# Kernel tuning notes

Hardware: AMD Instinct MI355X
Metric: run time of the kernel (lower is better)

Reference implementation:

```python
import jax, jax.numpy as jnp
import numpy as np
from jax.scipy.special import logsumexp

WORD_DIM = 512
SCRF_DIM = 256
N_TAGS = 12
ALLOWED_SPAN = 8
START_ID = 10
STOP_ID = 11
SEQ_LEN = 768
N_SPANS = 96


def _compute_scores(h, Wl, bl, Wr, br, Gl, bgl, Gr, bgr, Wt, bt, transitions):
    # h: [1, L, D] already projected by Dense
    Lc, D = h.shape[1], h.shape[2]
    scores = jnp.zeros((1, Lc, Lc, D), h.dtype)
    diag = jnp.arange(Lc)
    ht = h
    scores = scores.at[:, diag, diag].set(ht)
    for sl in range(1, min(ALLOWED_SPAN, Lc)):
        l, r = ht[:, :-1], ht[:, 1:]
        h_hat = 4.0 * jax.nn.sigmoid(l @ Wl.T + bl + r @ Wr.T + br) - 2.0
        # exp/normalize over 3 gates == softmax over gate axis
        g = (l @ Gl.T + bgl + r @ Gr.T + bgr).reshape(1, Lc - sl, 3, D)
        wgt = jax.nn.softmax(g, axis=2)
        ht = wgt[:, :, 0] * h_hat + wgt[:, :, 1] * l + wgt[:, :, 2] * r
        scores = scores.at[:, diag[:Lc - sl], diag[sl:]].set(ht)
    tagsc = scores @ Wt.T + bt  # [1, L, L, T]
    # final[b,i,j,prev,tag] = tagsc[b,i,j,tag] + transitions[prev,tag]
    return tagsc[:, :, :, None, :] + transitions[None, None, None]


def _forward_pass(s5):
    # s5: [1, L, L, T, T]; semi-Markov forward algorithm, windows of width <= ALLOWED_SPAN
    Lc, T = s5.shape[1], s5.shape[3]
    A = ALLOWED_SPAN
    i0 = jnp.arange(1, Lc + 1)
    k = jnp.arange(A)
    p = i0[:, None] - A + k[None, :]              # candidate span-start positions [L, A]
    m = p >= 0                                    # valid window mask (istarts = max(0, i-A))
    x = s5[0][jnp.clip(p, 0), (i0 - 1)[:, None]]  # [L, A, T, T] span scores ending at i-1
    buf0 = jnp.full((A, T), -10000.0, s5.dtype).at[A - 1, START_ID].set(0.0)

    def step(buf, inp):
        xi, mi = inp
        # tmp[k, prev, tag] = score + logalpha[start, prev]
        tmp = jnp.where(mi[:, None, None], xi + buf[:, :, None], -1e30)
        na = logsumexp(tmp, axis=(0, 1))  # [T]
        return jnp.concatenate([buf[1:], na[None]], axis=0), na

    _, alphas = jax.lax.scan(step, buf0, (x, m))
    return alphas[-1, :STOP_ID].sum()


def _gold_score(s5, tags):
    Lc, T = s5.shape[1], s5.shape[3]
    gf = tags[:, :, 0] * (Lc * T * T) + tags[:, :, 1] * (T * T) + tags[:, :, 2] * T + tags[:, :, 3]
    return jnp.take_along_axis(s5.reshape(1, -1), gf, axis=1).sum()


def setup_inputs() -> dict:
    key = jax.random.key(0)
    ks = jax.random.split(key, 16)
    D, W3 = SCRF_DIM, 3 * SCRF_DIM
    s = 0.05
    def w(k, shape):
        return jax.random.normal(k, shape, dtype=jnp.float32) * s
    return {
        "feats": jax.random.normal(ks[0], (1, SEQ_LEN, WORD_DIM), dtype=jnp.float32),
        "tags": jax.random.randint(ks[1], (1, N_SPANS, 4), 0, N_TAGS),
        "Wd": w(ks[2], (D, WORD_DIM)), "bd": jnp.zeros((D,), jnp.float32),
        "Wl": w(ks[3], (D, D)), "bl": jnp.zeros((D,), jnp.float32),
        "Wr": w(ks[4], (D, D)), "br": jnp.zeros((D,), jnp.float32),
        "Gl": w(ks[5], (W3, D)), "bgl": jnp.zeros((W3,), jnp.float32),
        "Gr": w(ks[6], (W3, D)), "bgr": jnp.zeros((W3,), jnp.float32),
        "Wt": w(ks[7], (N_TAGS, D)), "bt": jnp.zeros((N_TAGS,), jnp.float32),
        "transitions": w(ks[8], (N_TAGS, N_TAGS)),
    }


def reference(feats, tags, Wd, bd, Wl, bl, Wr, br, Gl, bgl, Gr, bgr, Wt, bt, transitions):
    h = feats @ Wd.T + bd  # Dense: word_dim -> scrf_dim
    s5 = _compute_scores(h, Wl, bl, Wr, br, Gl, bgl, Gr, bgr, Wt, bt, transitions)
    gold = _gold_score(s5, tags)
    logZ = _forward_pass(s5)
    return logZ - gold
```

## Files before the change

### kernel.cpp

```cpp
#include <hip/hip_runtime.h>

typedef __attribute__((ext_vector_type(8))) short short8;
typedef __attribute__((ext_vector_type(4))) float f32x4;

#define TPAD 100
#define BARSTRIDE 512

__device__ __forceinline__ float bf2f(short s) {
  return __uint_as_float(((unsigned)(unsigned short)s) << 16);
}
__device__ __forceinline__ unsigned short f2bf(float f) {
  unsigned u = __float_as_uint(f);
  unsigned rounding = 0x7fffu + ((u >> 16) & 1u);
  return (unsigned short)((u + rounding) >> 16);
}

__device__ __forceinline__ void stg_f32(float* p, float v) {
  asm volatile("global_store_dword %0, %1, off sc1" :: "v"(p), "v"(v) : "memory");
}
__device__ __forceinline__ void stg_u16(unsigned short* p, unsigned short v) {
  unsigned w = v;
  asm volatile("global_store_short %0, %1, off sc1" :: "v"(p), "v"(w) : "memory");
}

union __align__(16) SmemU {
  struct { unsigned short As[64][72]; unsigned short Ws[64][72]; float Cs[64][64]; } g;
  struct { unsigned short rows[2][8][264]; float sred[2][96]; float smu[2]; } bn;
  struct { float Bs[96 * TPAD]; float Acs[96 * TPAD]; float red[8]; } t;
  struct { float Qs[2][96 * TPAD]; float vv[4][96]; float red[8]; float redm[4]; } f;
};

__device__ __forceinline__ void bar_arrive(unsigned* bar, int nb) {
  asm volatile("s_waitcnt vmcnt(0) lgkmcnt(0)" ::: "memory");
  __syncthreads();
  if (threadIdx.x == 0) {
    int bid = blockIdx.x;
    int g = bid >> 5;
    int gsz = nb - (g << 5); if (gsz > 32) gsz = 32;
    unsigned gt = atomicAdd(&bar[g * 32], 1u);
    if ((int)gt == gsz - 1) atomicAdd(&bar[256], 1u);
  }
}
__device__ __forceinline__ void bar_wait(unsigned* bar, int nb) {
  int ngroups = (nb + 31) >> 5;
  if (threadIdx.x == 0) {
    while (__hip_atomic_load(&bar[256], __ATOMIC_RELAXED, __HIP_MEMORY_SCOPE_AGENT)
           < (unsigned)ngroups)
      __builtin_amdgcn_s_sleep(2);
  }
  __syncthreads();
}

__global__ void prep_kernel(const float* __restrict__ feats, const float* __restrict__ Wd,
                            const float* __restrict__ Wl, const float* __restrict__ Wr,
                            const float* __restrict__ Gl, const float* __restrict__ Gr,
                            const float* __restrict__ bl, const float* __restrict__ br,
                            const float* __restrict__ bgl, const float* __restrict__ bgr,
                            unsigned short* __restrict__ featsB, unsigned short* __restrict__ WdB,
                            unsigned short* __restrict__ WcB, float* __restrict__ bc,
                            unsigned* __restrict__ bars)
{
  int idx = blockIdx.x * 256 + threadIdx.x;
  if (idx < 393216) {
    featsB[idx] = f2bf(feats[idx]);
  } else if (idx < 524288) {
    int j = idx - 393216;
    WdB[j] = f2bf(Wd[j]);
  } else if (idx < 1048576) {
    int j = idx - 524288;
    int o = j >> 9, k = j & 511;
    float v;
    if (k < 256) v = (o < 256) ? Wl[o*256 + k] : Gl[(o-256)*256 + k];
    else { int k2 = k - 256; v = (o < 256) ? Wr[o*256 + k2] : Gr[(o-256)*256 + k2]; }
    WcB[j] = f2bf(v);
  } else if (idx < 1049600) {
    int o = idx - 1048576;
    bc[o] = (o < 256) ? bl[o] + br[o] : bgl[o-256] + bgr[o-256];
  } else {
    int j = idx - 1049600;
    if (j < 14 * BARSTRIDE) bars[j] = 0u;
  }
}

__device__ __forceinline__ void treelevel(SmemU& sm,
    const float* Tin, const float* Cin, float* Tout, float* Cout)
{
  const int bid = blockIdx.x;
  const int tid = threadIdx.x;
  const int wv = tid >> 6, lane = tid & 63;
  const int j = bid >> 1;
  const int cs = (bid & 1) * 48;
  const float* Ag = Tin + (size_t)(2*j) * 9216;
  const float* Bg = Tin + (size_t)(2*j + 1) * 9216;

  float4 av[9], bv[9];
  const float* ap = Ag + tid * 36;
  const float* bp = Bg + tid * 36;
  #pragma unroll
  for (int q = 0; q < 9; ++q) av[q] = *(const float4*)(ap + q*4);
  #pragma unroll
  for (int q = 0; q < 9; ++q) bv[q] = *(const float4*)(bp + q*4);
  float ma = 0.f, mb = 0.f;
  #pragma unroll
  for (int q = 0; q < 9; ++q) {
    ma = fmaxf(ma, fmaxf(fmaxf(av[q].x, av[q].y), fmaxf(av[q].z, av[q].w)));
    mb = fmaxf(mb, fmaxf(fmaxf(bv[q].x, bv[q].y), fmaxf(bv[q].z, bv[q].w)));
  }
  #pragma unroll
  for (int off = 32; off; off >>= 1) {
    ma = fmaxf(ma, __shfl_down(ma, off));
    mb = fmaxf(mb, __shfl_down(mb, off));
  }
  if (lane == 0) { sm.t.red[wv] = ma; sm.t.red[4 + wv] = mb; }
  __syncthreads();
  float fa = fmaxf(fmaxf(sm.t.red[0], sm.t.red[1]), fmaxf(sm.t.red[2], sm.t.red[3]));
  float fb = fmaxf(fmaxf(sm.t.red[4], sm.t.red[5]), fmaxf(sm.t.red[6], sm.t.red[7]));
  float ia = 1.0f / fa, ib = 1.0f / fb;

  #pragma unroll
  for (int q = 0; q < 9; ++q) {
    int e = tid*36 + q*4;
    int r = e / 96, k = e - r*96;
    float4 bb = bv[q];
    bb.x *= ib; bb.y *= ib; bb.z *= ib; bb.w *= ib;
    *(float4*)&sm.t.Bs[r*TPAD + k] = bb;
    float4 aa = av[q];
    sm.t.Acs[(k+0)*TPAD + r] = aa.x * ia;
    sm.t.Acs[(k+1)*TPAD + r] = aa.y * ia;
    sm.t.Acs[(k+2)*TPAD + r] = aa.z * ia;
    sm.t.Acs[(k+3)*TPAD + r] = aa.w * ia;
  }
  __syncthreads();

  int tr = tid >> 4, tc = tid & 15;
  int r0 = tr * 6, c0 = cs + tc * 3;
  float acc[6][3];
  #pragma unroll
  for (int i = 0; i < 6; ++i)
    #pragma unroll
    for (int m = 0; m < 3; ++m) acc[i][m] = 0.f;
  for (int k = 0; k < 96; k += 4) {
    float4 a0 = *(const float4*)&sm.t.Acs[(c0+0)*TPAD + k];
    float4 a1 = *(const float4*)&sm.t.Acs[(c0+1)*TPAD + k];
    float4 a2 = *(const float4*)&sm.t.Acs[(c0+2)*TPAD + k];
    #pragma unroll
    for (int i = 0; i < 6; ++i) {
      float4 b = *(const float4*)&sm.t.Bs[(r0+i)*TPAD + k];
      acc[i][0] += b.x*a0.x + b.y*a0.y + b.z*a0.z + b.w*a0.w;
      acc[i][1] += b.x*a1.x + b.y*a1.y + b.z*a1.z + b.w*a1.w;
      acc[i][2] += b.x*a2.x + b.y*a2.y + b.z*a2.z + b.w*a2.w;
    }
  }
  float* op = Tout + (size_t)j * 9216;
  #pragma unroll
  for (int i = 0; i < 6; ++i)
    #pragma unroll
    for (int m = 0; m < 3; ++m)
      stg_f32(&op[(size_t)(r0+i)*96 + c0 + m], acc[i][m]);
  if ((bid & 1) == 0 && tid == 0)
    stg_f32(&Cout[j], Cin[2*j] + Cin[2*j + 1] + __logf(fa) + __logf(fb));
}

__global__ __launch_bounds__(256, 2) void mega_kernel(
    const unsigned short* featsB, const unsigned short* WdB,
    const float* bd, const unsigned short* WcB, const float* bc,
    unsigned short* ht, const float* Wt, const float* bt,
    float* Bband, float* Xn, float* muv, const float* trans,
    const int* tags,
    float* T0, float* T1, float* T2, float* T3, float* T4,
    float* C0, float* C1, float* C2, float* C3, float* C4,
    float* out, unsigned* bars)
{
  __shared__ SmemU sm;
  const int bid = blockIdx.x;
  const int tid = threadIdx.x;
  const int wave = tid >> 6, lane = tid & 63;

  if (bid >= 192) {
    bar_wait(bars + 7*BARSTRIDE, 192);
  } else {
    if (bid < 48) {
      const int p0 = (bid % 12) * 64;
      const int n0 = (bid / 12) * 64;
      f32x4 acc[4];
      #pragma unroll
      for (int i = 0; i < 4; ++i)
        #pragma unroll
        for (int j = 0; j < 4; ++j) acc[i][j] = 0.f;
      const int lr = tid >> 3;
      const int c8 = (tid & 7) * 8;
      for (int kt = 0; kt < 8; ++kt) {
        int kb = kt * 64;
        #pragma unroll
        for (int rr = 0; rr < 64; rr += 32) {
          int row = lr + rr;
          *(short8*)(&sm.g.As[row][c8]) = *(const short8*)(featsB + (size_t)(p0 + row)*512 + kb + c8);
          *(short8*)(&sm.g.Ws[row][c8]) = *(const short8*)(WdB + (size_t)(n0 + row)*512 + kb + c8);
        }
        __syncthreads();
        int q8 = (lane >> 4) * 8;
        #pragma unroll
        for (int kk = 0; kk < 2; ++kk) {
          short8 bfr = *(const short8*)(&sm.g.Ws[wave*16 + (lane & 15)][kk*32 + q8]);
          #pragma unroll
          for (int mt = 0; mt < 4; ++mt) {
            short8 afr = *(const short8*)(&sm.g.As[mt*16 + (lane & 15)][kk*32 + q8]);
            acc[mt] = __builtin_amdgcn_mfma_f32_16x16x32_bf16(afr, bfr, acc[mt], 0, 0, 0);
          }
        }
        __syncthreads();
      }
      int o = n0 + wave*16 + (lane & 15);
      float bias = bd[o];
      #pragma unroll
      for (int mt = 0; mt < 4; ++mt)
        #pragma unroll
        for (int r = 0; r < 4; ++r) {
          int row = p0 + mt*16 + (lane >> 4)*4 + r;
          stg_u16(&ht[row*256 + o], f2bf(acc[mt][r] + bias));
        }
    }
    bar_arrive(bars + 0*BARSTRIDE, 192);
    bar_wait(bars + 0*BARSTRIDE, 192);

    for (int sl = 1; sl <= 7; ++sl) {
      {
        const unsigned short* htp = ht + (size_t)(sl - 1) * 196608;
        unsigned short* htn = ht + (size_t)sl * 196608;
        const int Mvalid = 768 - sl;
        const int p0 = (bid % 12) * 64;
        const int n0 = (bid / 12) * 16;
        f32x4 acc[4];
        #pragma unroll
        for (int i = 0; i < 4; ++i)
          #pragma unroll
          for (int j = 0; j < 4; ++j) acc[i][j] = 0.f;
        const int lr = tid >> 3;
        const int c8 = (tid & 7) * 8;
        for (int kt = 0; kt < 8; ++kt) {
          int kb = kt * 64;
          int shift = kb >> 8;
          int kcol = kb & 255;
          #pragma unroll
          for (int rr = 0; rr < 64; rr += 32) {
            int row = lr + rr;
            int grow = p0 + row + shift; if (grow > 767) grow = 767;
            *(short8*)(&sm.g.As[row][c8]) = *(const short8*)(htp + (size_t)grow*256 + kcol + c8);
            int o = (row >> 4)*256 + n0 + (row & 15);
            *(short8*)(&sm.g.Ws[row][c8]) = *(const short8*)(WcB + (size_t)o*512 + kb + c8);
          }
          __syncthreads();
          int q8 = (lane >> 4) * 8;
          #pragma unroll
          for (int kk = 0; kk < 2; ++kk) {
            short8 bfr = *(const short8*)(&sm.g.Ws[wave*16 + (lane & 15)][kk*32 + q8]);
            #pragma unroll
            for (int mt = 0; mt < 4; ++mt) {
              short8 afr = *(const short8*)(&sm.g.As[mt*16 + (lane & 15)][kk*32 + q8]);
              acc[mt] = __builtin_amdgcn_mfma_f32_16x16x32_bf16(afr, bfr, acc[mt], 0, 0, 0);
            }
          }
          __syncthreads();
        }
        #pragma unroll
        for (int mt = 0; mt < 4; ++mt)
          #pragma unroll
          for (int r = 0; r < 4; ++r)
            sm.g.Cs[mt*16 + (lane >> 4)*4 + r][wave*16 + (lane & 15)] = acc[mt][r];
        __syncthreads();

        int dl = tid & 15;
        int d = n0 + dl;
        float bz = bc[d], b0 = bc[256 + d], b1 = bc[512 + d], b2v = bc[768 + d];
        for (int pr = tid >> 4; pr < 64; pr += 16) {
          int p = p0 + pr;
          if (p >= Mvalid) continue;
          float z  = sm.g.Cs[pr][dl]      + bz;
          float g0 = sm.g.Cs[pr][16 + dl] + b0;
          float g1 = sm.g.Cs[pr][32 + dl] + b1;
          float g2 = sm.g.Cs[pr][48 + dl] + b2v;
          float l = bf2f((short)htp[p*256 + d]);
          float r = bf2f((short)htp[(p+1)*256 + d]);
          float hh = 4.f / (1.f + __expf(-z)) - 2.f;
          float mg = fmaxf(g0, fmaxf(g1, g2));
          float e0 = __expf(g0 - mg), e1 = __expf(g1 - mg), e2 = __expf(g2 - mg);
          float inv = 1.f / (e0 + e1 + e2);
          stg_u16(&htn[p*256 + d], f2bf((e0*hh + e1*l + e2*r) * inv));
        }
      }
      bar_arrive(bars + sl*BARSTRIDE, 192);
      bar_wait(bars + sl*BARSTRIDE, 192);
    }
  }

  for (int task = bid; task < 384; task += 256) {
    const int half = tid >> 7;
    const int t2 = tid & 127;
    const int i = 2*task + 1 + half;
    for (int q = t2; q < 256; q += 128) {
      int k = q >> 5, cc = (q & 31) * 8;
      int p = i - 8 + k;
      short8 v;
      if (p >= 0) {
        int slx = 7 - k;
        v = *(const short8*)(ht + ((size_t)slx*768 + p)*256 + cc);
      } else {
        #pragma unroll
        for (int j = 0; j < 8; ++j) v[j] = 0;
      }
      *(short8*)(&sm.bn.rows[half][k][cc]) = v;
    }
    __syncthreads();
    float res = -1e30f;
    if (t2 < 96) {
      int t = t2 >> 3, k = t2 & 7;
      int p = i - 8 + k;
      if (p >= 0) {
        float acc = 0.f;
        for (int dch = 0; dch < 256; dch += 8) {
          float4 wa = *(const float4*)(Wt + t*256 + dch);
          float4 wb = *(const float4*)(Wt + t*256 + dch + 4);
          short8 hv = *(const short8*)(&sm.bn.rows[half][k][dch]);
          acc += wa.x*bf2f(hv[0]) + wa.y*bf2f(hv[1]) + wa.z*bf2f(hv[2]) + wa.w*bf2f(hv[3])
               + wb.x*bf2f(hv[4]) + wb.y*bf2f(hv[5]) + wb.z*bf2f(hv[6]) + wb.w*bf2f(hv[7]);
        }
        res = acc + bt[t];
      }
      stg_f32(&Bband[(size_t)i*96 + t2], res);
      sm.bn.sred[half][t2] = res;
    }
    __syncthreads();
    if (t2 < 32) {
      float m = fmaxf(sm.bn.sred[half][t2],
                 fmaxf(sm.bn.sred[half][t2+32], sm.bn.sred[half][t2+64]));
      #pragma unroll
      for (int off = 16; off; off >>= 1) m = fmaxf(m, __shfl_down(m, off));
      if (t2 == 0) { stg_f32(&muv[i], m); sm.bn.smu[half] = m; }
    }
    __syncthreads();
    if (t2 < 96) stg_f32(&Xn[(size_t)i*96 + t2], __expf(res - sm.bn.smu[half]));
    __syncthreads();
  }
  bar_arrive(bars + 8*BARSTRIDE, 256);
  if (bid >= 240) return;
  bar_wait(bars + 8*BARSTRIDE, 256);

  {
    const int chunk = bid / 5;
    const int bxx = bid % 5;
    if (bxx == 0 && tid == 0) stg_f32(&C0[chunk], 0.f);
    const int a = chunk * 16;
    const int g = lane / 12;
    const int t = lane - g * 12;
    const int cidx = bxx * 20 + wave * 5 + g;
    const bool active = (g < 5) && (cidx < 96);
    const int c = active ? cidx : 95;
    const int s = c / 12, tau = c - s * 12;
    float Etc[12];
    #pragma unroll
    for (int jj = 0; jj < 12; ++jj) Etc[jj] = __expf(trans[jj*12 + t]);
    float NA[8], V[8];
    #pragma unroll
    for (int jj = 0; jj < 8; ++jj) { NA[jj] = 0.f; V[jj] = 0.f; }
    #pragma unroll
    for (int jj = 0; jj < 8; ++jj) if (jj == s) {
      NA[jj] = (t == tau) ? 1.f : 0.f;
      V[jj]  = Etc[tau];
    }
    const int gbb = (g * 12) * 4;
    #pragma unroll
    for (int m = 1; m <= 16; ++m) {
      const float* xr = Xn + (size_t)(a + m) * 96 + t * 8;
      float4 x0 = *(const float4*)xr;
      float4 x1 = *(const float4*)(xr + 4);
      float sf = __expf(-muv[a + m]);
      float na = x0.x*V[0] + x0.y*V[1] + x0.z*V[2] + x0.w*V[3]
               + x1.x*V[4] + x1.y*V[5] + x1.z*V[6] + x1.w*V[7];
      int nai = __float_as_int(na);
      float nb[12];
      #pragma unroll
      for (int jj = 0; jj < 12; ++jj)
        nb[jj] = __int_as_float(__builtin_amdgcn_ds_bpermute(gbb + jj*4, nai));
      float pp0 = nb[0]*Etc[0] + nb[1]*Etc[1] + nb[2]*Etc[2]   + nb[3]*Etc[3];
      float pp1 = nb[4]*Etc[4] + nb[5]*Etc[5] + nb[6]*Etc[6]   + nb[7]*Etc[7];
      float pp2 = nb[8]*Etc[8] + nb[9]*Etc[9] + nb[10]*Etc[10] + nb[11]*Etc[11];
      float v = (pp0 + pp1) + pp2;
      #pragma unroll
      for (int kq = 0; kq < 7; ++kq) { NA[kq] = NA[kq+1]*sf; V[kq] = V[kq+1]*sf; }
      NA[7] = na; V[7] = v;
    }
    if (active) {
      float* dst = T0 + (size_t)chunk * 9216 + c;
      #pragma unroll
      for (int jj = 0; jj < 8; ++jj) stg_f32(&dst[(size_t)(jj*12 + t) * 96], NA[jj]);
    }
  }
  bar_arrive(bars + 9*BARSTRIDE, 240);
  if (bid >= 48) return;
  bar_wait(bars + 9*BARSTRIDE, 240);

  treelevel(sm, T0, C0, T1, C1);
  bar_arrive(bars + 10*BARSTRIDE, 48);
  if (bid >= 24) return;
  bar_wait(bars + 10*BARSTRIDE, 48);
  treelevel(sm, T1, C1, T2, C2);
  bar_arrive(bars + 11*BARSTRIDE, 24);
  if (bid >= 12) return;
  bar_wait(bars + 11*BARSTRIDE, 24);
  treelevel(sm, T2, C2, T3, C3);
  bar_arrive(bars + 12*BARSTRIDE, 12);
  if (bid >= 6) return;
  bar_wait(bars + 12*BARSTRIDE, 12);
  treelevel(sm, T3, C3, T4, C4);
  bar_arrive(bars + 13*BARSTRIDE, 6);
  if (bid) return;
  bar_wait(bars + 13*BARSTRIDE, 6);

  {
    float4 P[9];
    const float* p0p = T4 + tid * 36;
    #pragma unroll
    for (int q = 0; q < 9; ++q) P[q] = *(const float4*)(p0p + q*4);

    float gold = 0.f;
    if (tid < 96) {
      int a = tags[tid*4+0], b = tags[tid*4+1], cc = tags[tid*4+2], d = tags[tid*4+3];
      float v = trans[cc*12 + d];
      int sl = b - a;
      if (sl >= 0 && sl < 8) v += Bband[(size_t)(b+1)*96 + d*8 + (7 - sl)];
      else v += bt[d];
      gold = v;
    }
    float mp = 0.f;
    for (int q = tid; q < 768; q += 256) mp += muv[1 + q];
    #pragma unroll
    for (int off = 32; off; off >>= 1) {
      gold += __shfl_down(gold, off);
      mp   += __shfl_down(mp, off);
    }
    if (lane == 0) { sm.f.red[wave] = gold; sm.f.red[4 + wave] = mp; }

    #pragma unroll
    for (int q = 0; q < 9; ++q) {
      int e = tid*36 + q*4;
      int r = e / 96, k = e - r*96;
      *(float4*)&sm.f.Qs[0][r*TPAD + k] = P[q];
    }
    if (tid < 96) sm.f.vv[0][tid] = (tid == 94) ? 1.f : 0.f;
    __syncthreads();
    float gold_t = sm.f.red[0] + sm.f.red[1] + sm.f.red[2] + sm.f.red[3];
    float musum  = sm.f.red[4] + sm.f.red[5] + sm.f.red[6] + sm.f.red[7];
    float Ct = C4[0] + C4[1] + C4[2];

    #pragma unroll
    for (int s = 0; s < 3; ++s) {
      if (s < 2) {
        const float* pn = T4 + (size_t)(s+1)*9216 + tid*36;
        #pragma unroll
        for (int q = 0; q < 9; ++q) P[q] = *(const float4*)(pn + q*4);
      }
      float acc = 0.f;
      if (tid < 96) {
        const float* Qr = &sm.f.Qs[s & 1][tid * TPAD];
        #pragma unroll
        for (int k = 0; k < 96; k += 4) {
          float4 qv = *(const float4*)(Qr + k);
          float4 zv = *(const float4*)&sm.f.vv[s][k];
          acc += qv.x*zv.x + qv.y*zv.y + qv.z*zv.z + qv.w*zv.w;
        }
      }
      float am = (tid < 96) ? acc : 0.f;
      #pragma unroll
      for (int off = 32; off; off >>= 1) am = fmaxf(am, __shfl_down(am, off));
      if (lane == 0) sm.f.redm[wave] = am;
      __syncthreads();
      float mx = fmaxf(fmaxf(sm.f.redm[0], sm.f.redm[1]), fmaxf(sm.f.redm[2], sm.f.redm[3]));
      Ct += __logf(mx);
      if (tid < 96) sm.f.vv[s+1][tid] = acc / mx;
      if (s < 2) {
        #pragma unroll
        for (int q = 0; q < 9; ++q) {
          int e = tid*36 + q*4;
          int r = e / 96, k = e - r*96;
          *(float4*)&sm.f.Qs[(s+1)&1][r*TPAD + k] = P[q];
        }
      }
      __syncthreads();
    }
    if (tid == 0) {
      float lsum = 0.f;
      #pragma unroll
      for (int t = 0; t < 11; ++t) lsum += __logf(sm.f.vv[3][84 + t]);
      out[0] = lsum + 11.f * (Ct + musum) - gold_t;
    }
  }
}

extern "C" void kernel_launch(void* const* d_in, const int* in_sizes, int n_in,
                              void* d_out, int out_size, void* d_ws, size_t ws_size,
                              hipStream_t stream)
{
  const float* feats = (const float*)d_in[0];
  const int*   tags  = (const int*)  d_in[1];
  const float* Wd    = (const float*)d_in[2];
  const float* bd    = (const float*)d_in[3];
  const float* Wl    = (const float*)d_in[4];
  const float* bl    = (const float*)d_in[5];
  const float* Wr    = (const float*)d_in[6];
  const float* br    = (const float*)d_in[7];
  const float* Gl    = (const float*)d_in[8];
  const float* bgl   = (const float*)d_in[9];
  const float* Gr    = (const float*)d_in[10];
  const float* bgr   = (const float*)d_in[11];
  const float* Wt    = (const float*)d_in[12];
  const float* bt    = (const float*)d_in[13];
  const float* trans = (const float*)d_in[14];
  float* out = (float*)d_out;

  char* ws = (char*)d_ws;
  unsigned short* featsB = (unsigned short*)(ws + 0);
  unsigned short* WdB    = (unsigned short*)(ws + 786432);
  unsigned short* WcB    = (unsigned short*)(ws + 1048576);
  float*          bc     = (float*)         (ws + 2097152);
  unsigned short* ht     = (unsigned short*)(ws + 2101248);
  float*          Bband  = (float*)         (ws + 5246976);
  float*          Xn     = (float*)         (ws + 5542272);
  float*          muv    = (float*)         (ws + 5837568);
  float*          T0     = (float*)         (ws + 5841664);
  float*          T1     = (float*)         (ws + 7611136);
  float*          T2     = (float*)         (ws + 8495872);
  float*          T3     = (float*)         (ws + 8938240);
  float*          T4     = (float*)         (ws + 9159424);
  float*          C0     = (float*)         (ws + 9270016);
  float*          C1     = (float*)         (ws + 9270272);
  float*          C2     = (float*)         (ws + 9270528);
  float*          C3     = (float*)         (ws + 9270784);
  float*          C4     = (float*)         (ws + 9271040);
  unsigned*       bars   = (unsigned*)      (ws + 9271296);

  prep_kernel<<<4128, 256, 0, stream>>>(feats, Wd, Wl, Wr, Gl, Gr, bl, br, bgl, bgr,
                                        featsB, WdB, WcB, bc, bars);
  mega_kernel<<<256, 256, 0, stream>>>(featsB, WdB, bd, WcB, bc, ht, Wt, bt,
                                       Bband, Xn, muv, trans, tags,
                                       T0, T1, T2, T3, T4, C0, C1, C2, C3, C4,
                                       out, bars);
}
```

Measured before the change: 225.8 us.

## Replace grid-wide barriers with fine-grained per-tile dependency flags

Removes the global atomic barriers between stages of the persistent mega-kernel and has blocks wait only on counters for the specific row tiles, tasks or tree nodes they read. Each span-length step now waits only on its own and the neighbouring row tile from the previous step, letting work flow as a wavefront rather than stopping for the whole grid. This cuts idle time at barriers but adds more spinning atomics, a larger flag array to zero in the prep kernel, and a spin timeout that could break correctness if it is ever hit.

Measured after the change: 219.9 us. -2.6%, faster.

```diff
diff --git a/kernel.cpp b/kernel.cpp
--- a/kernel.cpp
+++ b/kernel.cpp
@@ -4,7 +4,6 @@
 typedef __attribute__((ext_vector_type(4))) float f32x4;
 
 #define TPAD 100
-#define BARSTRIDE 512
 
 __device__ __forceinline__ float bf2f(short s) {
   return __uint_as_float(((unsigned)(unsigned short)s) << 16);
@@ -22,6 +21,16 @@
   unsigned w = v;
   asm volatile("global_store_short %0, %1, off sc1" :: "v"(p), "v"(w) : "memory");
 }
+
+#define NFLAGS 18432
+__device__ __forceinline__ void flag_spin(unsigned* f, unsigned tgt) {
+  unsigned n = 0;
+  while (__hip_atomic_load(f, __ATOMIC_RELAXED, __HIP_MEMORY_SCOPE_AGENT) < tgt) {
+    __builtin_amdgcn_s_sleep(2);
+    if (++n > 2000000u) break;
+  }
+}
+#define DRAIN() asm volatile("s_waitcnt vmcnt(0) lgkmcnt(0)" ::: "memory")
 
 union __align__(16) SmemU {
   struct { unsigned short As[64][72]; unsigned short Ws[64][72]; float Cs[64][64]; } g;
@@ -29,27 +38,6 @@
   struct { float Bs[96 * TPAD]; float Acs[96 * TPAD]; float red[8]; } t;
   struct { float Qs[2][96 * TPAD]; float vv[4][96]; float red[8]; float redm[4]; } f;
 };
-
-__device__ __forceinline__ void bar_arrive(unsigned* bar, int nb) {
-  asm volatile("s_waitcnt vmcnt(0) lgkmcnt(0)" ::: "memory");
-  __syncthreads();
-  if (threadIdx.x == 0) {
-    int bid = blockIdx.x;
-    int g = bid >> 5;
-    int gsz = nb - (g << 5); if (gsz > 32) gsz = 32;
-    unsigned gt = atomicAdd(&bar[g * 32], 1u);
-    if ((int)gt == gsz - 1) atomicAdd(&bar[256], 1u);
-  }
-}
-__device__ __forceinline__ void bar_wait(unsigned* bar, int nb) {
-  int ngroups = (nb + 31) >> 5;
-  if (threadIdx.x == 0) {
-    while (__hip_atomic_load(&bar[256], __ATOMIC_RELAXED, __HIP_MEMORY_SCOPE_AGENT)
-           < (unsigned)ngroups)
-      __builtin_amdgcn_s_sleep(2);
-  }
-  __syncthreads();
-}
 
 __global__ void prep_kernel(const float* __restrict__ feats, const float* __restrict__ Wd,
                             const float* __restrict__ Wl, const float* __restrict__ Wr,
@@ -58,7 +46,7 @@
                             const float* __restrict__ bgl, const float* __restrict__ bgr,
                             unsigned short* __restrict__ featsB, unsigned short* __restrict__ WdB,
                             unsigned short* __restrict__ WcB, float* __restrict__ bc,
-                            unsigned* __restrict__ bars)
+                            unsigned* __restrict__ flags)
 {
   int idx = blockIdx.x * 256 + threadIdx.x;
   if (idx < 393216) {
@@ -78,7 +66,7 @@
     bc[o] = (o < 256) ? bl[o] + br[o] : bgl[o-256] + bgr[o-256];
   } else {
     int j = idx - 1049600;
-    if (j < 14 * BARSTRIDE) bars[j] = 0u;
+    if (j < NFLAGS) flags[j] = 0u;
   }
 }
 
@@ -169,18 +157,17 @@
     const int* tags,
     float* T0, float* T1, float* T2, float* T3, float* T4,
     float* C0, float* C1, float* C2, float* C3, float* C4,
-    float* out, unsigned* bars)
+    float* out, unsigned* flags)
 {
   __shared__ SmemU sm;
   const int bid = blockIdx.x;
   const int tid = threadIdx.x;
   const int wave = tid >> 6, lane = tid & 63;
 
-  if (bid >= 192) {
-    bar_wait(bars + 7*BARSTRIDE, 192);
-  } else {
+  if (bid < 192) {
+    const int p = bid % 12;
     if (bid < 48) {
-      const int p0 = (bid % 12) * 64;
+      const int p0 = p * 64;
       const int n0 = (bid / 12) * 64;
       f32x4 acc[4];
       #pragma unroll
@@ -219,16 +206,23 @@
           int row = p0 + mt*16 + (lane >> 4)*4 + r;
           stg_u16(&ht[row*256 + o], f2bf(acc[mt][r] + bias));
         }
-    }
-    bar_arrive(bars + 0*BARSTRIDE, 192);
-    bar_wait(bars + 0*BARSTRIDE, 192);
+      DRAIN();
+      __syncthreads();
+      if (tid == 0) atomicAdd(&flags[(0*12 + p)*32], 1u);
+    }
 
     for (int sl = 1; sl <= 7; ++sl) {
+      unsigned tgt = (sl == 1) ? 4u : 16u;
+      if (tid == 0) {
+        flag_spin(&flags[((sl-1)*12 + p)*32], tgt);
+        if (p < 11) flag_spin(&flags[((sl-1)*12 + p + 1)*32], tgt);
+      }
+      __syncthreads();
       {
         const unsigned short* htp = ht + (size_t)(sl - 1) * 196608;
         unsigned short* htn = ht + (size_t)sl * 196608;
         const int Mvalid = 768 - sl;
-        const int p0 = (bid % 12) * 64;
+        const int p0 = p * 64;
         const int n0 = (bid / 12) * 16;
         f32x4 acc[4];
         #pragma unroll
@@ -273,37 +267,45 @@
         int d = n0 + dl;
         float bz = bc[d], b0 = bc[256 + d], b1 = bc[512 + d], b2v = bc[768 + d];
         for (int pr = tid >> 4; pr < 64; pr += 16) {
-          int p = p0 + pr;
-          if (p >= Mvalid) continue;
+          int pw = p0 + pr;
+          if (pw >= Mvalid) continue;
           float z  = sm.g.Cs[pr][dl]      + bz;
           float g0 = sm.g.Cs[pr][16 + dl] + b0;
           float g1 = sm.g.Cs[pr][32 + dl] + b1;
           float g2 = sm.g.Cs[pr][48 + dl] + b2v;
-          float l = bf2f((short)htp[p*256 + d]);
-          float r = bf2f((short)htp[(p+1)*256 + d]);
+          float l = bf2f((short)htp[pw*256 + d]);
+          float r = bf2f((short)htp[(pw+1)*256 + d]);
           float hh = 4.f / (1.f + __expf(-z)) - 2.f;
           float mg = fmaxf(g0, fmaxf(g1, g2));
           float e0 = __expf(g0 - mg), e1 = __expf(g1 - mg), e2 = __expf(g2 - mg);
           float inv = 1.f / (e0 + e1 + e2);
-          stg_u16(&htn[p*256 + d], f2bf((e0*hh + e1*l + e2*r) * inv));
-        }
-      }
-      bar_arrive(bars + sl*BARSTRIDE, 192);
-      bar_wait(bars + sl*BARSTRIDE, 192);
+          stg_u16(&htn[pw*256 + d], f2bf((e0*hh + e1*l + e2*r) * inv));
+        }
+      }
+      DRAIN();
+      __syncthreads();
+      if (tid == 0) atomicAdd(&flags[(sl*12 + p)*32], 1u);
     }
   }
 
   for (int task = bid; task < 384; task += 256) {
+    if (tid == 0) {
+      int rlo = 2*task - 7; if (rlo < 0) rlo = 0;
+      int tlo = rlo >> 6, thi = (2*task + 1) >> 6;
+      flag_spin(&flags[(7*12 + tlo)*32], 16u);
+      if (thi != tlo) flag_spin(&flags[(7*12 + thi)*32], 16u);
+    }
+    __syncthreads();
     const int half = tid >> 7;
     const int t2 = tid & 127;
     const int i = 2*task + 1 + half;
     for (int q = t2; q < 256; q += 128) {
       int k = q >> 5, cc = (q & 31) * 8;
-      int p = i - 8 + k;
+      int pr = i - 8 + k;
       short8 v;
-      if (p >= 0) {
+      if (pr >= 0) {
         int slx = 7 - k;
-        v = *(const short8*)(ht + ((size_t)slx*768 + p)*256 + cc);
+        v = *(const short8*)(ht + ((size_t)slx*768 + pr)*256 + cc);
       } else {
         #pragma unroll
         for (int j = 0; j < 8; ++j) v[j] = 0;
@@ -314,8 +316,8 @@
     float res = -1e30f;
     if (t2 < 96) {
       int t = t2 >> 3, k = t2 & 7;
-      int p = i - 8 + k;
-      if (p >= 0) {
+      int pr = i - 8 + k;
+      if (pr >= 0) {
         float acc = 0.f;
         for (int dch = 0; dch < 256; dch += 8) {
           float4 wa = *(const float4*)(Wt + t*256 + dch);
@@ -339,15 +341,21 @@
     }
     __syncthreads();
     if (t2 < 96) stg_f32(&Xn[(size_t)i*96 + t2], __expf(res - sm.bn.smu[half]));
-    __syncthreads();
-  }
-  bar_arrive(bars + 8*BARSTRIDE, 256);
+    DRAIN();
+    __syncthreads();
+    if (tid == 0) atomicAdd(&flags[(96 + task)*32], 1u);
+  }
   if (bid >= 240) return;
-  bar_wait(bars + 8*BARSTRIDE, 256);
 
   {
     const int chunk = bid / 5;
     const int bxx = bid % 5;
+    if (tid == 0) {
+      #pragma unroll
+      for (int q = 0; q < 8; ++q)
+        flag_spin(&flags[(96 + 8*chunk + q)*32], 1u);
+    }
+    __syncthreads();
     if (bxx == 0 && tid == 0) stg_f32(&C0[chunk], 0.f);
     const int a = chunk * 16;
     const int g = lane / 12;
@@ -394,29 +402,68 @@
       #pragma unroll
       for (int jj = 0; jj < 8; ++jj) stg_f32(&dst[(size_t)(jj*12 + t) * 96], NA[jj]);
     }
-  }
-  bar_arrive(bars + 9*BARSTRIDE, 240);
+    DRAIN();
+    __syncthreads();
+    if (tid == 0) atomicAdd(&flags[(480 + chunk)*32], 1u);
+  }
   if (bid >= 48) return;
-  bar_wait(bars + 9*BARSTRIDE, 240);
-
-  treelevel(sm, T0, C0, T1, C1);
-  bar_arrive(bars + 10*BARSTRIDE, 48);
+
+  {
+    int j = bid >> 1;
+    if (tid == 0) {
+      flag_spin(&flags[(480 + 2*j    )*32], 5u);
+      flag_spin(&flags[(480 + 2*j + 1)*32], 5u);
+    }
+    __syncthreads();
+    treelevel(sm, T0, C0, T1, C1);
+    DRAIN(); __syncthreads();
+    if (tid == 0) atomicAdd(&flags[(528 + j)*32], 1u);
+  }
   if (bid >= 24) return;
-  bar_wait(bars + 10*BARSTRIDE, 48);
-  treelevel(sm, T1, C1, T2, C2);
-  bar_arrive(bars + 11*BARSTRIDE, 24);
+  {
+    int j = bid >> 1;
+    if (tid == 0) {
+      flag_spin(&flags[(528 + 2*j    )*32], 2u);
+      flag_spin(&flags[(528 + 2*j + 1)*32], 2u);
+    }
+    __syncthreads();
+    treelevel(sm, T1, C1, T2, C2);
+    DRAIN(); __syncthreads();
+    if (tid == 0) atomicAdd(&flags[(552 + j)*32], 1u);
+  }
   if (bid >= 12) return;
-  bar_wait(bars + 11*BARSTRIDE, 24);
-  treelevel(sm, T2, C2, T3, C3);
-  bar_arrive(bars + 12*BARSTRIDE, 12);
+  {
+    int j = bid >> 1;
+    if (tid == 0) {
+      flag_spin(&flags[(552 + 2*j    )*32], 2u);
+      flag_spin(&flags[(552 + 2*j + 1)*32], 2u);
+    }
+    __syncthreads();
+    treelevel(sm, T2, C2, T3, C3);
+    DRAIN(); __syncthreads();
+    if (tid == 0) atomicAdd(&flags[(564 + j)*32], 1u);
+  }
   if (bid >= 6) return;
-  bar_wait(bars + 12*BARSTRIDE, 12);
-  treelevel(sm, T3, C3, T4, C4);
-  bar_arrive(bars + 13*BARSTRIDE, 6);
+  {
+    int j = bid >> 1;
+    if (tid == 0) {
+      flag_spin(&flags[(564 + 2*j    )*32], 2u);
+      flag_spin(&flags[(564 + 2*j + 1)*32], 2u);
+    }
+    __syncthreads();
+    treelevel(sm, T3, C3, T4, C4);
+    DRAIN(); __syncthreads();
+    if (tid == 0) atomicAdd(&flags[(570 + j)*32], 1u);
+  }
   if (bid) return;
-  bar_wait(bars + 13*BARSTRIDE, 6);
 
   {
+    if (tid == 0) {
+      flag_spin(&flags[(570)*32], 2u);
+      flag_spin(&flags[(571)*32], 2u);
+      flag_spin(&flags[(572)*32], 2u);
+    }
+    __syncthreads();
     float4 P[9];
     const float* p0p = T4 + tid * 36;
     #pragma unroll
@@ -536,12 +583,12 @@
   float*          C2     = (float*)         (ws + 9270528);
   float*          C3     = (float*)         (ws + 9270784);
   float*          C4     = (float*)         (ws + 9271040);
-  unsigned*       bars   = (unsigned*)      (ws + 9271296);
-
-  prep_kernel<<<4128, 256, 0, stream>>>(feats, Wd, Wl, Wr, Gl, Gr, bl, br, bgl, bgr,
-                                        featsB, WdB, WcB, bc, bars);
+  unsigned*       flags  = (unsigned*)      (ws + 9271296);
+
+  prep_kernel<<<4172, 256, 0, stream>>>(feats, Wd, Wl, Wr, Gl, Gr, bl, br, bgl, bgr,
+                                        featsB, WdB, WcB, bc, flags);
   mega_kernel<<<256, 256, 0, stream>>>(featsB, WdB, bd, WcB, bc, ht, Wt, bt,
                                        Bband, Xn, muv, trans, tags,
                                        T0, T1, T2, T3, T4, C0, C1, C2, C3, C4,
-                                       out, bars);
-}
+                                       out, flags);
+}
```
